# Optimization experiments

Measured on AMD Instinct MI355X. Metric: run time of the kernel, lower is better.

## Reference

```python
import jax, jax.numpy as jnp
import numpy as np
import math

N_NODES, CHANNELS, N_ELEM, N_FEAT = 4096, 128, 10, 128
LS_IN = [0, 1, 2]          # input irreps per channel: 0e+1o+2e -> dim 9
L_OUT = [0, 1]             # keep_irrep_out = {0e, 1o}
L12_MAX = 3                # cap on intermediate coupling
SLICES = {0: (0, 1), 1: (1, 4), 2: (4, 9)}
PATHS1 = [l for l in L_OUT if l in LS_IN]
PATHS2 = [(l1, l2, lo) for l1 in LS_IN for l2 in LS_IN for lo in L_OUT if abs(l1 - l2) <= lo <= l1 + l2]
T12_KEYS = [(l1, l2, l12) for l1 in LS_IN for l2 in LS_IN for l12 in range(abs(l1 - l2), min(l1 + l2, L12_MAX) + 1)]
PATHS3 = [(k, l3, lo) for k in T12_KEYS for l3 in LS_IN for lo in L_OUT if abs(k[2] - l3) <= lo <= k[2] + l3]

def _su2_cg(j1, m1, j2, m2, j3, m3):
    if m3 != m1 + m2:
        return 0.0
    f = math.factorial
    vmin = max(-j1 + j2 + m3, -j1 + m1, 0)
    vmax = min(j2 + j3 + m1, j3 - j1 + j2, j3 + m3)
    C = math.sqrt((2 * j3 + 1) * f(j3 + j1 - j2) * f(j3 - j1 + j2) * f(j1 + j2 - j3) * f(j3 + m3) * f(j3 - m3)
                  / (f(j1 + j2 + j3 + 1) * f(j1 - m1) * f(j1 + m1) * f(j2 - m2) * f(j2 + m2)))
    S = 0.0
    for v in range(vmin, vmax + 1):
        S += (-1) ** (v + j2 + m2) * f(j2 + j3 + m1 - v) * f(j1 - m1 + v) / (
            f(v) * f(j3 - j1 + j2 - v) * f(j3 + m3 - v) * f(v + j1 - j2 - m3))
    return C * S

def _c2r(l):
    # change of basis real -> complex spherical harmonics (e3nn convention)
    q = np.zeros((2 * l + 1, 2 * l + 1), dtype=np.complex128)
    for m in range(-l, 0):
        q[l + m, l + abs(m)] = 1.0 / math.sqrt(2)
        q[l + m, l - abs(m)] = -1j / math.sqrt(2)
    q[l, l] = 1.0
    for m in range(1, l + 1):
        q[l + m, l + abs(m)] = (-1) ** m / math.sqrt(2)
        q[l + m, l - abs(m)] = 1j * (-1) ** m / math.sqrt(2)
    return (-1j) ** l * q

_CG = {}
def real_cg(l1, l2, l3):
    key = (l1, l2, l3)
    if key not in _CG:
        Cc = np.zeros((2 * l1 + 1, 2 * l2 + 1, 2 * l3 + 1), dtype=np.complex128)
        for i, m1 in enumerate(range(-l1, l1 + 1)):
            for j, m2 in enumerate(range(-l2, l2 + 1)):
                for k, m3 in enumerate(range(-l3, l3 + 1)):
                    Cc[i, j, k] = _su2_cg(l1, m1, l2, m2, l3, m3)
        R = np.einsum('ij,kl,mn,ikn->jlm', _c2r(l1), _c2r(l2), np.conj(_c2r(l3).T), Cc)
        _CG[key] = np.real(R).astype(np.float32)
    return _CG[key]

def setup_inputs():
    key = jax.random.key(0)
    k = jax.random.split(key, 8)
    node_feats = jax.random.normal(k[0], (N_NODES, CHANNELS, 9), dtype=jnp.float32)
    species = jax.random.randint(k[1], (N_NODES,), 0, N_ELEM)
    w1 = jax.random.normal(k[2], (N_ELEM, len(PATHS1), CHANNELS), dtype=jnp.float32) / math.sqrt(len(PATHS1))
    w2 = jax.random.normal(k[3], (N_ELEM, len(PATHS2), CHANNELS), dtype=jnp.float32) / math.sqrt(len(PATHS2))
    w3 = jax.random.normal(k[4], (N_ELEM, len(PATHS3), CHANNELS), dtype=jnp.float32) / math.sqrt(len(PATHS3))
    lin_w0 = jax.random.normal(k[5], (CHANNELS, N_FEAT), dtype=jnp.float32)
    lin_w1 = jax.random.normal(k[6], (CHANNELS, N_FEAT), dtype=jnp.float32)
    return {"node_feats": node_feats, "w1": w1, "w2": w2, "w3": w3,
            "lin_w0": lin_w0, "lin_w1": lin_w1, "species": species}

def reference(node_feats, w1, w2, w3, lin_w0, lin_w1, species):
    n, c = node_feats.shape[:2]
    attrs = jax.nn.one_hot(species, N_ELEM, dtype=node_feats.dtype)
    A = {l: node_feats[..., SLICES[l][0]:SLICES[l][1]] for l in LS_IN}
    # element-dependent path weights per node
    w1n = jnp.einsum('ne,epc->npc', attrs, w1)
    w2n = jnp.einsum('ne,epc->npc', attrs, w2)
    w3n = jnp.einsum('ne,epc->npc', attrs, w3)
    B = {lo: jnp.zeros((n, c, 2 * lo + 1), node_feats.dtype) for lo in L_OUT}
    # correlation order 1
    for p, lo in enumerate(PATHS1):
        B[lo] = B[lo] + w1n[:, p, :, None] * A[lo]
    for p, (l1, l2, lo) in enumerate(PATHS2):
        cg = jnp.asarray(real_cg(l1, l2, lo))
        t = jnp.einsum('ijk,nci,ncj->nck', cg, A[l1], A[l2])
        B[lo] = B[lo] + w2n[:, p, :, None] * t
    T12 = {}
    for kk in T12_KEYS:
        l1, l2, l12 = kk
        T12[kk] = jnp.einsum('ijk,nci,ncj->nck', jnp.asarray(real_cg(l1, l2, l12)), A[l1], A[l2])
    for p, (kk, l3, lo) in enumerate(PATHS3):
        cg = jnp.asarray(real_cg(kk[2], l3, lo))
        t = jnp.einsum('ijk,nci,ncj->nck', cg, T12[kk], A[l3])
        B[lo] = B[lo] + w3n[:, p, :, None] * t
    # equivariant Linear: mix channel axis into num_features per output irrep
    s = 1.0 / math.sqrt(c)
    out0 = jnp.einsum('ncm,cf->nfm', B[0], lin_w0) * s
    out1 = jnp.einsum('ncm,cf->nfm', B[1], lin_w1) * s
    return jnp.concatenate([out0, out1], axis=-1)  # [N, F, 1+3]
```

## Files before the change

### kernel.cpp

```cpp
#include <hip/hip_runtime.h>
#include <utility>


#define NN 4096
#define NC 128

template<typename F, int... Is>
__device__ __forceinline__ void sfor_impl(F&& f, std::integer_sequence<int, Is...>) {
  (f(std::integral_constant<int, Is>{}), ...);
}
template<int N, typename F>
__device__ __forceinline__ void sfor(F&& f) {
  sfor_impl((F&&)f, std::make_integer_sequence<int, N>{});
}

constexpr int T_L1c[19]  = {0,0,0,1,1,1,1,1,1,1,2,2,2,2,2,2,2,2,3};
constexpr int T_L2c[19]  = {0,1,2,0,1,1,1,2,2,2,0,1,1,1,2,2,2,2,2};
constexpr int T_L3c[19]  = {0,1,2,1,0,1,2,1,2,3,2,1,2,3,0,1,2,3,1};
constexpr int T_OFFc[19] = {0,1,10,35,44,53,80,125,170,245,350,375,420,495,600,625,700,825,1000};
constexpr int AOFFc[3]   = {0,1,4};

constexpr int P2_L1c[9]  = {0,0,1,1,1,1,2,2,2};
constexpr int P2_L2c[9]  = {0,1,0,1,1,2,1,2,2};
constexpr int P2_LOc[9]  = {0,1,1,0,1,1,1,0,1};
constexpr int P2_TBLc[9] = {0,1,3,4,5,7,11,14,15};

constexpr int K_L1c[18]  = {0,0,0,1,1,1,1,1,1,1,2,2,2,2,2,2,2,2};
constexpr int K_L2c[18]  = {0,1,2,0,1,1,1,2,2,2,0,1,1,1,2,2,2,2};
constexpr int K_L12c[18] = {0,1,2,1,0,1,2,1,2,3,2,1,2,3,0,1,2,3};

constexpr int P3_STARTc[19] = {0,2,6,9,13,15,19,22,26,29,30,33,37,40,41,43,47,50,51};
constexpr int P3_L3c[51] = {
  0,1,  0,1,1,2,  1,2,2,  0,1,1,2,  0,1,  0,1,1,2,  1,2,2,  0,1,1,2,  1,2,2,
  2,  1,2,2,  0,1,1,2,  1,2,2,  2,  0,1,  0,1,1,2,  1,2,2,  2 };
constexpr int P3_LOc[51] = {
  0,1,  1,0,1,1,  1,0,1,  1,0,1,1,  0,1,  1,0,1,1,  1,0,1,  1,0,1,1,  1,0,1,
  1,  1,0,1,  1,0,1,1,  1,0,1,  1,  0,1,  1,0,1,1,  1,0,1,  1 };
constexpr int P3_TBLc[51] = {
  0,1,  3,4,5,7,  11,14,15,  3,4,5,7,  0,1,  3,4,5,7,  11,14,15,  3,4,5,7,
  11,14,15,  18,  11,14,15,  3,4,5,7,  11,14,15,  18,  0,1,  3,4,5,7,
  11,14,15,  18 };

constexpr double cfact(int n) { double r = 1.0; for (int i = 2; i <= n; ++i) r *= i; return r; }
constexpr double csqrt(double x) {
  if (x <= 0.0) return 0.0;
  double r = x > 1.0 ? x : 1.0;
  for (int i = 0; i < 64; ++i) r = 0.5 * (r + x / r);
  return r;
}
constexpr double su2cg(int j1, int m1, int j2, int m2, int j3, int m3) {
  if (m3 != m1 + m2) return 0.0;
  int vmin = -j1 + j2 + m3; if (-j1 + m1 > vmin) vmin = -j1 + m1; if (vmin < 0) vmin = 0;
  int vmax = j2 + j3 + m1; if (j3 - j1 + j2 < vmax) vmax = j3 - j1 + j2; if (j3 + m3 < vmax) vmax = j3 + m3;
  double C = csqrt((2.0 * j3 + 1.0)
                   * cfact(j3 + j1 - j2) * cfact(j3 - j1 + j2) * cfact(j1 + j2 - j3)
                   * cfact(j3 + m3) * cfact(j3 - m3)
                   / (cfact(j1 + j2 + j3 + 1) * cfact(j1 - m1) * cfact(j1 + m1)
                      * cfact(j2 - m2) * cfact(j2 + m2)));
  double S = 0.0;
  for (int v = vmin; v <= vmax; ++v) {
    double sgn = ((v + j2 + m2) & 1) ? -1.0 : 1.0;
    S += sgn * cfact(j2 + j3 + m1 - v) * cfact(j1 - m1 + v)
         / (cfact(v) * cfact(j3 - j1 + j2 - v) * cfact(j3 + m3 - v) * cfact(v + j1 - j2 - m3));
  }
  return C * S;
}

struct Cx { double re, im; };
constexpr Cx cxmul(Cx a, Cx b) { return Cx{a.re * b.re - a.im * b.im, a.re * b.im + a.im * b.re}; }
struct Row { int cnt; int col[2]; Cx v[2]; };

constexpr Row c2r_row(int l, int r) {
  Row out{0, {0, 0}, {{0, 0}, {0, 0}}};
  constexpr double is2 = 0.70710678118654752440;
  const int m = r - l;
  if (m < 0) {
    out.cnt = 2;
    out.col[0] = l - m; out.v[0] = Cx{is2, 0.0};
    out.col[1] = l + m; out.v[1] = Cx{0.0, -is2};
  } else if (m == 0) {
    out.cnt = 1; out.col[0] = l; out.v[0] = Cx{1.0, 0.0};
  } else {
    const double sgn = (m & 1) ? -1.0 : 1.0;
    out.cnt = 2;
    out.col[0] = l + m; out.v[0] = Cx{sgn * is2, 0.0};
    out.col[1] = l - m; out.v[1] = Cx{0.0, sgn * is2};
  }
  const int ph = l & 3;
  for (int a = 0; a < out.cnt; ++a) {
    Cx v = out.v[a];
    out.v[a] = (ph == 0) ? v
             : (ph == 1) ? Cx{v.im, -v.re}
             : (ph == 2) ? Cx{-v.re, -v.im}
                         : Cx{-v.im, v.re};
  }
  return out;
}

struct CGAll { float v[1105]; };
constexpr CGAll make_cg() {
  CGAll R{};
  for (int t = 0; t < 19; ++t) {
    const int l1 = T_L1c[t], l2 = T_L2c[t], l3 = T_L3c[t], off = T_OFFc[t];
    const int d1 = 2 * l1 + 1, d2 = 2 * l2 + 1, d3 = 2 * l3 + 1;
    double tmp[175] = {};
    for (int i = 0; i < d1; ++i) {
      const int m1 = i - l1;
      const Row r1 = c2r_row(l1, i);
      for (int k = 0; k < d2; ++k) {
        const int m2 = k - l2, m3 = m1 + m2;
        if (m3 < -l3 || m3 > l3) continue;
        const double cc = su2cg(l1, m1, l2, m2, l3, m3);
        if (cc == 0.0) continue;
        const Row r2 = c2r_row(l2, k);
        const Row r3 = c2r_row(l3, m3 + l3);
        for (int a = 0; a < r1.cnt; ++a)
          for (int b = 0; b < r2.cnt; ++b) {
            const Cx q12 = cxmul(r1.v[a], r2.v[b]);
            for (int cdx = 0; cdx < r3.cnt; ++cdx) {
              const double re = q12.re * r3.v[cdx].re + q12.im * r3.v[cdx].im;
              tmp[(r1.col[a] * d2 + r2.col[b]) * d3 + r3.col[cdx]] += re * cc;
            }
          }
      }
    }
    const int sz = d1 * d2 * d3;
    for (int e = 0; e < sz; ++e) R.v[off + e] = (float)tmp[e];
  }
  return R;
}
constexpr CGAll CG_ALL = make_cg();

__global__ __launch_bounds__(128) void epb_main(
    const float* __restrict__ nf,
    const float* __restrict__ w1,
    const float* __restrict__ w2,
    const float* __restrict__ w3,
    const float* __restrict__ lw0,
    const float* __restrict__ lw1,
    const int*   __restrict__ species,
    float* __restrict__ out)
{
  __shared__ float4 Anf4[288];
  __shared__ float4 Bsh[NC];
  const int n = blockIdx.x, c = threadIdx.x;

  const float4* src = reinterpret_cast<const float4*>(nf + (size_t)n * (NC * 9));
  Anf4[c]       = src[c];
  Anf4[c + 128] = src[c + 128];
  if (c < 32) Anf4[c + 256] = src[c + 256];
  const int s = species[n];
  __syncthreads();

  const float* Anf = reinterpret_cast<const float*>(Anf4);
  float A[9];
  #pragma unroll
  for (int i = 0; i < 9; ++i) A[i] = Anf[c * 9 + i];

  const float* w1p = w1 + (size_t)s * 2 * NC + c;
  const float* w2p = w2 + (size_t)s * 9 * NC + c;
  const float* w3p = w3 + (size_t)s * 51 * NC + c;

  float B[4] = {0.f, 0.f, 0.f, 0.f};

  {
    const float w10 = w1p[0];
    const float w11 = w1p[NC];
    B[0] = fmaf(w10, A[0], B[0]);
    B[1] = fmaf(w11, A[1], B[1]);
    B[2] = fmaf(w11, A[2], B[2]);
    B[3] = fmaf(w11, A[3], B[3]);
  }

  sfor<9>([&](auto P) {
    constexpr int p  = P.value;
    constexpr int l1 = P2_L1c[p], l2 = P2_L2c[p], lo = P2_LOc[p];
    constexpr int d1 = 2 * l1 + 1, d2 = 2 * l2 + 1, dl = 2 * lo + 1;
    constexpr int off = T_OFFc[P2_TBLc[p]];
    const float w = w2p[p * NC];
    sfor<dl>([&](auto Kk) {
      constexpr int k = Kk.value;
      float v = 0.f;
      sfor<d1>([&](auto I) {
        sfor<d2>([&](auto J) {
          constexpr float cgc = CG_ALL.v[off + (I.value * d2 + J.value) * dl + k];
          if constexpr (cgc != 0.0f) {
            constexpr int ia = AOFFc[l1] + I.value, ja = AOFFc[l2] + J.value;
            constexpr int x = ia < ja ? ia : ja, y = ia < ja ? ja : ia;
            v = fmaf(cgc, A[x] * A[y], v);
          }
        });
      });
      B[lo + k] = fmaf(w, v, B[lo + k]);
    });
  });

  sfor<18>([&](auto T) {
    constexpr int t   = T.value;
    constexpr int l1  = K_L1c[t], l2 = K_L2c[t], l12 = K_L12c[t];
    constexpr int d1  = 2 * l1 + 1, d2 = 2 * l2 + 1, d12 = 2 * l12 + 1;
    constexpr int off = T_OFFc[t];
    float tt[d12];
    sfor<d12>([&](auto Kk) {
      constexpr int k = Kk.value;
      float v = 0.f;
      sfor<d1>([&](auto I) {
        sfor<d2>([&](auto J) {
          constexpr float cgc = CG_ALL.v[off + (I.value * d2 + J.value) * d12 + k];
          if constexpr (cgc != 0.0f) {
            constexpr int ia = AOFFc[l1] + I.value, ja = AOFFc[l2] + J.value;
            constexpr int x = ia < ja ? ia : ja, y = ia < ja ? ja : ia;
            v = fmaf(cgc, A[x] * A[y], v);
          }
        });
      });
      tt[k] = v;
    });
    constexpr int pcnt = P3_STARTc[t + 1] - P3_STARTc[t];
    sfor<pcnt>([&](auto PP) {
      constexpr int p  = P3_STARTc[t] + PP.value;
      constexpr int l3 = P3_L3c[p], lo = P3_LOc[p];
      constexpr int d3 = 2 * l3 + 1, dl = 2 * lo + 1;
      constexpr int off2 = T_OFFc[P3_TBLc[p]];
      const float w = w3p[p * NC];
      sfor<dl>([&](auto M) {
        float v = 0.f;
        sfor<d12>([&](auto Kk) {
          sfor<d3>([&](auto J) {
            constexpr float cgc = CG_ALL.v[off2 + (Kk.value * d3 + J.value) * dl + M.value];
            if constexpr (cgc != 0.0f)
              v = fmaf(cgc, tt[Kk.value] * A[AOFFc[l3] + J.value], v);
          });
        });
        B[lo + M.value] = fmaf(w, v, B[lo + M.value]);
      });
    });
  });

  Bsh[c] = make_float4(B[0], B[1], B[2], B[3]);
  __syncthreads();

  const float scale = 0.08838834764831845f;
  const float* lw0p = lw0 + c;
  const float* lw1p = lw1 + c;
  float o0 = 0.f, o1 = 0.f, o2 = 0.f, o3 = 0.f;
  #pragma unroll 16
  for (int ch = 0; ch < NC; ++ch) {
    const float4 b = Bsh[ch];
    const float wa = lw0p[ch * NC];
    const float wb = lw1p[ch * NC];
    o0 = fmaf(b.x, wa, o0);
    o1 = fmaf(b.y, wb, o1);
    o2 = fmaf(b.z, wb, o2);
    o3 = fmaf(b.w, wb, o3);
  }
  const float4 r = make_float4(o0 * scale, o1 * scale, o2 * scale, o3 * scale);
  *reinterpret_cast<float4*>(out + (size_t)(n * NC + c) * 4) = r;
}

extern "C" void kernel_launch(void* const* d_in, const int* in_sizes, int n_in,
                              void* d_out, int out_size, void* d_ws, size_t ws_size,
                              hipStream_t stream) {
  const float* nf  = (const float*)d_in[0];
  const float* w1  = (const float*)d_in[1];
  const float* w2  = (const float*)d_in[2];
  const float* w3  = (const float*)d_in[3];
  const float* lw0 = (const float*)d_in[4];
  const float* lw1 = (const float*)d_in[5];
  const int*   spc = (const int*)  d_in[6];
  float* out = (float*)d_out;
  (void)d_ws; (void)ws_size; (void)in_sizes; (void)n_in; (void)out_size;

  hipLaunchKernelGGL(epb_main, dim3(NN), dim3(NC), 0, stream,
                     nf, w1, w2, w3, lw0, lw1, spc, out);
}
```

Before: 108.1 us.

## Process eight nodes per block and register-tile the channel-mixing linear

Each block now handles eight nodes with 256 threads. The symmetric-basis stage loops over four nodes per thread, and the final equivariant linear is register-tiled so each thread computes 2 nodes × 2 features. Each loaded lin_w value is reused across several nodes, which cuts repeated global/L2 reads of the 128x128 weight matrices that previously happened once per node. The cost is more shared memory per block (about 53KB) and higher register pressure, which may reduce occupancy, plus fewer blocks overall (512).

```diff
diff --git a/kernel.cpp b/kernel.cpp
--- a/kernel.cpp
+++ b/kernel.cpp
@@ -4,6 +4,7 @@
 
 #define NN 4096
 #define NC 128
+#define TN 8
 
 template<typename F, int... Is>
 __device__ __forceinline__ void sfor_impl(F&& f, std::integer_sequence<int, Is...>) {
@@ -131,37 +132,18 @@
 }
 constexpr CGAll CG_ALL = make_cg();
 
-__global__ __launch_bounds__(128) void epb_main(
-    const float* __restrict__ nf,
-    const float* __restrict__ w1,
-    const float* __restrict__ w2,
-    const float* __restrict__ w3,
-    const float* __restrict__ lw0,
-    const float* __restrict__ lw1,
-    const int*   __restrict__ species,
-    float* __restrict__ out)
+__device__ __forceinline__ void basis_pair(
+    const float* __restrict__ Ap,
+    const float* __restrict__ w1p,
+    const float* __restrict__ w2p,
+    const float* __restrict__ w3p,
+    float B[4])
 {
-  __shared__ float4 Anf4[288];
-  __shared__ float4 Bsh[NC];
-  const int n = blockIdx.x, c = threadIdx.x;
-
-  const float4* src = reinterpret_cast<const float4*>(nf + (size_t)n * (NC * 9));
-  Anf4[c]       = src[c];
-  Anf4[c + 128] = src[c + 128];
-  if (c < 32) Anf4[c + 256] = src[c + 256];
-  const int s = species[n];
-  __syncthreads();
-
-  const float* Anf = reinterpret_cast<const float*>(Anf4);
   float A[9];
   #pragma unroll
-  for (int i = 0; i < 9; ++i) A[i] = Anf[c * 9 + i];
-
-  const float* w1p = w1 + (size_t)s * 2 * NC + c;
-  const float* w2p = w2 + (size_t)s * 9 * NC + c;
-  const float* w3p = w3 + (size_t)s * 51 * NC + c;
-
-  float B[4] = {0.f, 0.f, 0.f, 0.f};
+  for (int i = 0; i < 9; ++i) A[i] = Ap[i];
+
+  B[0] = B[1] = B[2] = B[3] = 0.f;
 
   {
     const float w10 = w1p[0];
@@ -236,26 +218,82 @@
       });
     });
   });
-
-  Bsh[c] = make_float4(B[0], B[1], B[2], B[3]);
+}
+
+__global__ __launch_bounds__(256) void epb_main(
+    const float* __restrict__ nf,
+    const float* __restrict__ w1,
+    const float* __restrict__ w2,
+    const float* __restrict__ w3,
+    const float* __restrict__ lw0,
+    const float* __restrict__ lw1,
+    const int*   __restrict__ species,
+    float* __restrict__ out)
+{
+  __shared__ float  Anf[TN * NC * 9];
+  __shared__ float4 Bsh[TN * NC];
+  const int t  = threadIdx.x;
+  const int nb = blockIdx.x * TN;
+
+  {
+    const float4* src = reinterpret_cast<const float4*>(nf + (size_t)nb * (NC * 9));
+    float4* dst = reinterpret_cast<float4*>(Anf);
+    #pragma unroll
+    for (int i = 0; i < 9; ++i) dst[t + 256 * i] = src[t + 256 * i];
+  }
   __syncthreads();
 
-  const float scale = 0.08838834764831845f;
-  const float* lw0p = lw0 + c;
-  const float* lw1p = lw1 + c;
-  float o0 = 0.f, o1 = 0.f, o2 = 0.f, o3 = 0.f;
-  #pragma unroll 16
+  {
+    const int c = t & 127, h = t >> 7;
+    #pragma unroll 1
+    for (int q = 0; q < 4; ++q) {
+      const int nl = h + 2 * q;
+      const int s  = species[nb + nl];
+      const float* w1p = w1 + (size_t)s * 2  * NC + c;
+      const float* w2p = w2 + (size_t)s * 9  * NC + c;
+      const float* w3p = w3 + (size_t)s * 51 * NC + c;
+      float B[4];
+      basis_pair(Anf + nl * (NC * 9) + c * 9, w1p, w2p, w3p, B);
+      Bsh[nl * NC + c] = make_float4(B[0], B[1], B[2], B[3]);
+    }
+  }
+  __syncthreads();
+
+  const int fl = t & 63, g = t >> 6;
+  const float* pa = lw0 + fl;
+  const float* pb = lw1 + fl;
+  const float4* b0p = &Bsh[g * NC];
+  const float4* b1p = &Bsh[(g + 4) * NC];
+
+  float a00 = 0.f, a01 = 0.f, a02 = 0.f, a03 = 0.f;
+  float a10 = 0.f, a11 = 0.f, a12 = 0.f, a13 = 0.f;
+  float a20 = 0.f, a21 = 0.f, a22 = 0.f, a23 = 0.f;
+  float a30 = 0.f, a31 = 0.f, a32 = 0.f, a33 = 0.f;
+
+  #pragma unroll 8
   for (int ch = 0; ch < NC; ++ch) {
-    const float4 b = Bsh[ch];
-    const float wa = lw0p[ch * NC];
-    const float wb = lw1p[ch * NC];
-    o0 = fmaf(b.x, wa, o0);
-    o1 = fmaf(b.y, wb, o1);
-    o2 = fmaf(b.z, wb, o2);
-    o3 = fmaf(b.w, wb, o3);
-  }
-  const float4 r = make_float4(o0 * scale, o1 * scale, o2 * scale, o3 * scale);
-  *reinterpret_cast<float4*>(out + (size_t)(n * NC + c) * 4) = r;
+    const float wa0 = pa[ch * NC];
+    const float wa1 = pa[ch * NC + 64];
+    const float wb0 = pb[ch * NC];
+    const float wb1 = pb[ch * NC + 64];
+    const float4 b0 = b0p[ch];
+    const float4 b1 = b1p[ch];
+    a00 = fmaf(b0.x, wa0, a00); a01 = fmaf(b0.y, wb0, a01);
+    a02 = fmaf(b0.z, wb0, a02); a03 = fmaf(b0.w, wb0, a03);
+    a10 = fmaf(b0.x, wa1, a10); a11 = fmaf(b0.y, wb1, a11);
+    a12 = fmaf(b0.z, wb1, a12); a13 = fmaf(b0.w, wb1, a13);
+    a20 = fmaf(b1.x, wa0, a20); a21 = fmaf(b1.y, wb0, a21);
+    a22 = fmaf(b1.z, wb0, a22); a23 = fmaf(b1.w, wb0, a23);
+    a30 = fmaf(b1.x, wa1, a30); a31 = fmaf(b1.y, wb1, a31);
+    a32 = fmaf(b1.z, wb1, a32); a33 = fmaf(b1.w, wb1, a33);
+  }
+
+  const float s4 = 0.08838834764831845f;
+  float4* out4 = reinterpret_cast<float4*>(out);
+  out4[(size_t)(nb + g) * NC + fl]          = make_float4(a00*s4, a01*s4, a02*s4, a03*s4);
+  out4[(size_t)(nb + g) * NC + fl + 64]     = make_float4(a10*s4, a11*s4, a12*s4, a13*s4);
+  out4[(size_t)(nb + g + 4) * NC + fl]      = make_float4(a20*s4, a21*s4, a22*s4, a23*s4);
+  out4[(size_t)(nb + g + 4) * NC + fl + 64] = make_float4(a30*s4, a31*s4, a32*s4, a33*s4);
 }
 
 extern "C" void kernel_launch(void* const* d_in, const int* in_sizes, int n_in,
@@ -271,6 +309,6 @@
   float* out = (float*)d_out;
   (void)d_ws; (void)ws_size; (void)in_sizes; (void)n_in; (void)out_size;
 
-  hipLaunchKernelGGL(epb_main, dim3(NN), dim3(NC), 0, stream,
+  hipLaunchKernelGGL(epb_main, dim3(NN / TN), dim3(256), 0, stream,
                      nf, w1, w2, w3, lw0, lw1, spc, out);
 }
```

Result: no change. 107.6 us (-0.5%).
